# Optimization experiments

Hardware: AMD Instinct MI355X
Metric: run time of the kernel (lower is better)

## Reference

```python
import jax, jax.numpy as jnp
import numpy as np
import math

S, B, H, NH = 2048, 1, 4096, 32
HD = H // NH          # 128 head dim
ROT = HD // 2         # 64 rotary dim per half (position_encoding_2d)


def _rotary_tables(seq_len):
    inv_freq = 1.0 / (10000.0 ** (jnp.arange(0, ROT, 2, dtype=jnp.float32) / ROT))  # [ROT/2]
    t = jnp.arange(seq_len, dtype=jnp.float32)
    freqs = jnp.einsum('i,j->ij', t, inv_freq)          # [S, ROT/2]
    emb = jnp.concatenate([freqs, freqs], axis=-1)       # [S, ROT]
    return jnp.cos(emb), jnp.sin(emb)


def _rotate_half(x):
    half = x.shape[-1] // 2
    return jnp.concatenate([-x[..., half:], x[..., :half]], axis=-1)


def _apply_rotary(q, k, cos, sin, pos):
    # q,k: [s,b,nh,ROT]; pos: [s,b]
    c = cos[pos][:, :, None, :]   # [s,b,1,ROT]
    s_ = sin[pos][:, :, None, :]
    return q * c + _rotate_half(q) * s_, k * c + _rotate_half(k) * s_


def reference(hidden_states, position_ids, attention_mask, layer_id, w_qkv, b_qkv, w_dense, b_dense):
    s, b, _ = hidden_states.shape
    # fused QKV projection (Linear: x @ W.T + b)
    qkv = jnp.einsum('sbh,oh->sbo', hidden_states, w_qkv) + b_qkv     # [s,b,3H]
    qkv = qkv.reshape(s, b, NH, 3 * HD)
    q, k, v = jnp.split(qkv, 3, axis=-1)                               # each [s,b,nh,HD]
    # 2D rotary: split head dim in two halves, rotate with pos / block pos ids
    cos, sin = _rotary_tables(s)
    pos = position_ids[:, 0, :].T        # [s,b]
    blk = position_ids[:, 1, :].T        # [s,b]
    q1, q2 = jnp.split(q, 2, axis=-1)
    k1, k2 = jnp.split(k, 2, axis=-1)
    q1, k1 = _apply_rotary(q1, k1, cos, sin, pos)
    q2, k2 = _apply_rotary(q2, k2, cos, sin, blk)
    q = jnp.concatenate([q1, q2], axis=-1)
    k = jnp.concatenate([k1, k2], axis=-1)
    # layer-id-dependent scaling (GLM numerics): q scaled down by coeff, logits scaled back up
    coeff = float(layer_id + 1)
    q = q / (math.sqrt(HD) * coeff)
    scores = jnp.einsum('sbnd,tbnd->bnst', q, k)                       # [b,nh,s,s]
    scores = jnp.where(attention_mask, jnp.asarray(-10000.0, scores.dtype), scores)
    probs = jax.nn.softmax(scores.astype(jnp.float32) * coeff, axis=-1).astype(scores.dtype)
    ctx = jnp.einsum('bnst,tbnd->sbnd', probs, v).reshape(s, b, H)     # [s,b,H]
    return jnp.einsum('sbh,oh->sbo', ctx, w_dense) + b_dense


def setup_inputs() -> dict:
    key = jax.random.key(0)
    k1, k2, k3, k4, k5, k6 = jax.random.split(key, 6)
    init = 0.02
    hidden_states = jax.random.normal(k1, (S, B, H), dtype=jnp.float32)
    # GLM-style 2D position ids: [B, 2, S] (row 0: positions, row 1: block positions)
    pos = jnp.broadcast_to(jnp.arange(S, dtype=jnp.int64), (B, S))
    blk = jnp.broadcast_to(jnp.arange(S, dtype=jnp.int64), (B, S))
    position_ids = jnp.stack([pos, blk], axis=1)                        # [B,2,S]
    # causal mask: True = masked (future positions)
    causal = jnp.triu(jnp.ones((S, S), dtype=bool), k=1)
    attention_mask = jnp.broadcast_to(causal[None, None], (B, 1, S, S))
    return {
        'hidden_states': hidden_states,
        'position_ids': position_ids,
        'attention_mask': attention_mask,
        'layer_id': 5,
        'w_qkv': jax.random.normal(k2, (3 * H, H), dtype=jnp.float32) * init,
        'b_qkv': jax.random.normal(k3, (3 * H,), dtype=jnp.float32) * init,
        'w_dense': jax.random.normal(k4, (H, H), dtype=jnp.float32) * init,
        'b_dense': jax.random.normal(k5, (H,), dtype=jnp.float32) * init,
    }
```

## Files before the change

### kernel.cpp

```cpp
#include <hip/hip_runtime.h>
#include <math.h>
#include <stdint.h>

constexpr int S  = 2048;
constexpr int H  = 4096;
constexpr int NH = 32;
constexpr int HD = 128;
constexpr int H3 = 3 * H;

typedef unsigned short u16;
typedef __bf16 bf16x8 __attribute__((ext_vector_type(8)));
typedef float  f32x4  __attribute__((ext_vector_type(4)));
typedef unsigned short us8 __attribute__((ext_vector_type(8)));

__device__ __forceinline__ u16 f2bf(float f) {
  uint32_t u = __float_as_uint(f);
  uint32_t r = (u + 0x7fff + ((u >> 16) & 1)) >> 16;
  return (u16)r;
}
__device__ __forceinline__ float bf2f(u16 u) {
  return __uint_as_float((uint32_t)u << 16);
}

__device__ __forceinline__ void load_lds16(const void* g, void* l) {
  __builtin_amdgcn_global_load_lds(
      (__attribute__((address_space(1))) void*)(uintptr_t)g,
      (__attribute__((address_space(3))) void*)l,
      16, 0, 0);
}

#define SBAR0 __builtin_amdgcn_sched_barrier(0)

__global__ __launch_bounds__(256)
void cast_all(const float* __restrict__ w_qkv, const float* __restrict__ hidden,
              const float* __restrict__ w_dense, u16* __restrict__ wq,
              u16* __restrict__ hb, u16* __restrict__ wd) {
  constexpr int NQ  = H3 * H / 4;
  constexpr int NHd = S * H / 4;
  constexpr int ND  = H * H / 4;
  constexpr int NT  = NQ + NHd + ND;
  for (int i = blockIdx.x * 256 + threadIdx.x; i < NT; i += gridDim.x * 256) {
    const float4* src;
    ushort4* dst;
    int j = i;
    if (j < NQ)            { src = (const float4*)w_qkv;  dst = (ushort4*)wq; }
    else if (j < NQ + NHd) { j -= NQ; src = (const float4*)hidden; dst = (ushort4*)hb; }
    else                   { j -= NQ + NHd; src = (const float4*)w_dense; dst = (ushort4*)wd; }
    float4 v = src[j];
    ushort4 o;
    o.x = f2bf(v.x); o.y = f2bf(v.y); o.z = f2bf(v.z); o.w = f2bf(v.w);
    dst[j] = o;
  }
}

template<int NCOLS, int OUT_BF16>
__global__ __launch_bounds__(512, 2)
void gemm8p(const u16* __restrict__ A, const u16* __restrict__ W,
            const float* __restrict__ bias, void* __restrict__ Cout) {
  constexpr int K  = 4096;
  constexpr int NT = K / 64;
  constexpr int NTM = 16;
  constexpr int TB = 49152;
  __shared__ __attribute__((aligned(16))) unsigned char lds[3 * TB];
  const int tid = threadIdx.x, wave = tid >> 6, lane = tid & 63;
  const int l15 = lane & 15, l4 = lane >> 4;
  const int wr = wave >> 2, wc = wave & 3;

  const int nwg = gridDim.x, bid = blockIdx.x;
  const int cpx = nwg >> 3;
  const int swz = (bid & 7) * cpx + (bid >> 3);
  const int bx = swz / NTM, by = swz - bx * NTM;
  const int bm = by * 128, bn = bx * 256;

  const int srow = lane >> 3;
  const int sck  = ((lane & 7) ^ srow) * 8;
  const u16* Abase = A + (size_t)(bm + srow) * K + sck;
  const u16* Wbase = W + (size_t)(bn + srow) * K + sck;

  auto stageA = [&](int tt, int b) {
#pragma unroll
    for (int j = 0; j < 2; ++j) {
      const int rb = j * 64 + wave * 8;
      load_lds16(Abase + (size_t)rb * K + tt * 64, &lds[b * TB + rb * 128]);
    }
  };
  auto stageB = [&](int tt, int b, int u) {
#pragma unroll
    for (int j = 0; j < 2; ++j) {
      const int rb = u * 128 + j * 64 + wave * 8;
      load_lds16(Wbase + (size_t)rb * K + tt * 64,
                 &lds[b * TB + 16384 + rb * 128]);
    }
  };

  f32x4 acc[4][4];
#pragma unroll
  for (int i = 0; i < 4; ++i)
#pragma unroll
    for (int j = 0; j < 4; ++j) acc[i][j] = (f32x4)0.f;

  stageA(0, 0); stageB(0, 0, 0); stageB(0, 0, 1);
  stageA(1, 1); stageB(1, 1, 0); stageB(1, 1, 1);
  asm volatile("s_waitcnt vmcnt(6)" ::: "memory");
  SBAR0;
  __builtin_amdgcn_s_barrier();

  const int arow = wr * 64 + l15;
  const int brow = wc * 64 + l15;
  const int ckx  = l15 & 7;

  bf16x8 af[4][2], bf[4][2];

  int br = 0, bs = 2;
  for (int t = 0; t < NT; ++t) {
    const int b0 = br * TB;
#pragma unroll
    for (int mi = 0; mi < 2; ++mi)
#pragma unroll
      for (int ks = 0; ks < 2; ++ks)
        af[mi][ks] = *(const bf16x8*)&lds[b0 + (arow + mi * 16) * 128 +
                                          (((ks * 4 + l4) ^ ckx) * 16)];
#pragma unroll
    for (int ni = 0; ni < 2; ++ni)
#pragma unroll
      for (int ks = 0; ks < 2; ++ks)
        bf[ni][ks] = *(const bf16x8*)&lds[b0 + 16384 + (brow + ni * 16) * 128 +
                                          (((ks * 4 + l4) ^ ckx) * 16)];
    if (t < NT - 2) stageA(t + 2, bs);
    SBAR0; __builtin_amdgcn_s_barrier();
    asm volatile("s_waitcnt lgkmcnt(0)" ::: "memory");
    SBAR0;
    __builtin_amdgcn_s_setprio(1);
#pragma unroll
    for (int ks = 0; ks < 2; ++ks)
#pragma unroll
      for (int mi = 0; mi < 2; ++mi)
#pragma unroll
        for (int ni = 0; ni < 2; ++ni)
          acc[mi][ni] = __builtin_amdgcn_mfma_f32_16x16x32_bf16(af[mi][ks], bf[ni][ks], acc[mi][ni], 0, 0, 0);
    __builtin_amdgcn_s_setprio(0);
    SBAR0; __builtin_amdgcn_s_barrier();
#pragma unroll
    for (int ni = 2; ni < 4; ++ni)
#pragma unroll
      for (int ks = 0; ks < 2; ++ks)
        bf[ni][ks] = *(const bf16x8*)&lds[b0 + 16384 + (brow + ni * 16) * 128 +
                                          (((ks * 4 + l4) ^ ckx) * 16)];
    if (t < NT - 2) stageB(t + 2, bs, 0);
    SBAR0; __builtin_amdgcn_s_barrier();
    asm volatile("s_waitcnt lgkmcnt(0)" ::: "memory");
    SBAR0;
    __builtin_amdgcn_s_setprio(1);
#pragma unroll
    for (int ks = 0; ks < 2; ++ks)
#pragma unroll
      for (int mi = 0; mi < 2; ++mi)
#pragma unroll
        for (int ni = 2; ni < 4; ++ni)
          acc[mi][ni] = __builtin_amdgcn_mfma_f32_16x16x32_bf16(af[mi][ks], bf[ni][ks], acc[mi][ni], 0, 0, 0);
    __builtin_amdgcn_s_setprio(0);
    SBAR0; __builtin_amdgcn_s_barrier();
#pragma unroll
    for (int mi = 2; mi < 4; ++mi)
#pragma unroll
      for (int ks = 0; ks < 2; ++ks)
        af[mi][ks] = *(const bf16x8*)&lds[b0 + (arow + mi * 16) * 128 +
                                          (((ks * 4 + l4) ^ ckx) * 16)];
    if (t < NT - 2) stageB(t + 2, bs, 1);
    SBAR0; __builtin_amdgcn_s_barrier();
    asm volatile("s_waitcnt lgkmcnt(0)" ::: "memory");
    SBAR0;
    __builtin_amdgcn_s_setprio(1);
#pragma unroll
    for (int ks = 0; ks < 2; ++ks)
#pragma unroll
      for (int mi = 2; mi < 4; ++mi)
#pragma unroll
        for (int ni = 0; ni < 2; ++ni)
          acc[mi][ni] = __builtin_amdgcn_mfma_f32_16x16x32_bf16(af[mi][ks], bf[ni][ks], acc[mi][ni], 0, 0, 0);
    __builtin_amdgcn_s_setprio(0);
    SBAR0; __builtin_amdgcn_s_barrier();
    __builtin_amdgcn_s_setprio(1);
#pragma unroll
    for (int ks = 0; ks < 2; ++ks)
#pragma unroll
      for (int mi = 2; mi < 4; ++mi)
#pragma unroll
        for (int ni = 2; ni < 4; ++ni)
          acc[mi][ni] = __builtin_amdgcn_mfma_f32_16x16x32_bf16(af[mi][ks], bf[ni][ks], acc[mi][ni], 0, 0, 0);
    __builtin_amdgcn_s_setprio(0);
    if (t < NT - 1) {
      if (t < NT - 2) asm volatile("s_waitcnt vmcnt(6)" ::: "memory");
      else            asm volatile("s_waitcnt vmcnt(0)" ::: "memory");
      SBAR0;
      __builtin_amdgcn_s_barrier();
    }
    br = (br == 2) ? 0 : br + 1;
    bs = (bs == 2) ? 0 : bs + 1;
  }

#pragma unroll
  for (int ni = 0; ni < 4; ++ni) {
    const int col = bn + wc * 64 + ni * 16 + l15;
    const float bv = bias[col];
#pragma unroll
    for (int mi = 0; mi < 4; ++mi) {
#pragma unroll
      for (int r = 0; r < 4; ++r) {
        const int row = bm + wr * 64 + mi * 16 + l4 * 4 + r;
        const float v = acc[mi][ni][r] + bv;
        if (OUT_BF16) ((u16*)Cout)[(size_t)row * NCOLS + col] = f2bf(v);
        else          ((float*)Cout)[(size_t)row * NCOLS + col] = v;
      }
    }
  }
}

__global__ __launch_bounds__(256)
void rotary_fused(const u16* __restrict__ qkv,
                  u16* __restrict__ Qb, u16* __restrict__ Kb,
                  u16* __restrict__ Vt) {
  __shared__ u16 vt[64][136];
  __shared__ float2 cs_tab[64][32];
  const int s0 = blockIdx.x * 64, h = blockIdx.y;
  const int tid = threadIdx.x;

  for (int idx = tid; idx < 2048; idx += 256) {
    const int r = idx >> 5, j = idx & 31;
    const float invf = exp2f(-(float)j * (13.287712379549449f / 32.f));
    float sn, c;
    sincosf((float)(s0 + r) * invf, &sn, &c);
    cs_tab[r][j] = make_float2(c, sn);
  }
  for (int idx = tid; idx < 1024; idx += 256) {
    const int r = idx >> 4, ck = idx & 15;
    us8 v = *(const us8*)(qkv + (size_t)(s0 + r) * H3 + h * 384 + 256 + ck * 8);
    *(us8*)&vt[r][ck * 8] = v;
  }
  __syncthreads();

  for (int idx = tid; idx < 2048; idx += 256) {
    const int r  = idx >> 5;
    const int sub = idx & 31;
    const int tq = sub >> 4;
    const int ck = sub & 15;
    const int s = s0 + r;
    const u16* base = qkv + (size_t)s * H3 + h * 384 + tq * 128;
    us8 v = *(const us8*)(base + ck * 8);
    us8 p = *(const us8*)(base + ((ck * 8) ^ 32));
    const int d0 = ck * 8;
    const float sign = ((d0 & 63) < 32) ? -1.f : 1.f;
    const float sc = tq ? 1.f : 0.12751721769218683f;
    us8 o;
#pragma unroll
    for (int e = 0; e < 8; ++e) {
      const float2 cs = cs_tab[r][(d0 + e) & 31];
      o[e] = f2bf((bf2f(v[e]) * cs.x + sign * bf2f(p[e]) * cs.y) * sc);
    }
    *(us8*)((tq ? Kb : Qb) + ((size_t)h * S + s) * HD + d0) = o;
  }
  for (int idx = tid; idx < 1024; idx += 256) {
    const int d = idx >> 3, c8 = idx & 7;
    us8 o;
#pragma unroll
    for (int e = 0; e < 8; ++e) o[e] = vt[c8 * 8 + e][d];
    *(us8*)(Vt + ((size_t)h * HD + d) * S + s0 + c8 * 8) = o;
  }
}

__global__ __launch_bounds__(256)
void attn(const u16* __restrict__ Qb, const u16* __restrict__ Kb,
          const u16* __restrict__ Vt, u16* __restrict__ ctx) {
  __shared__ __attribute__((aligned(16))) unsigned char sK[2][64 * 256];
  __shared__ __attribute__((aligned(16))) unsigned char sV[2][128 * 128];
  __shared__ __attribute__((aligned(16))) unsigned char sP[4][16 * 128];
  const int bid = blockIdx.x;
  const int ixd = bid >> 3;
  const int h   = (bid & 7) * 4 + (ixd >> 5);
  const int qb  = 31 - (ixd & 31);
  const int tid = threadIdx.x, wave = tid >> 6, lane = tid & 63;
  const int l15 = lane & 15, l4 = lane >> 4;
  const int qw0 = qb * 64 + wave * 16;

  auto stage = [&](int it) {
    const int t0 = it * 64, b = it & 1;
#pragma unroll
    for (int c = 0; c < 4; ++c) {
      const int rbase = c * 16 + wave * 4;
      const int rr = rbase + (lane >> 4);
      const int p = lane & 15;
      load_lds16(Kb + ((size_t)h * S + t0 + rr) * HD + ((p ^ (rr & 15)) * 8),
                 &sK[b][rbase * 256]);
    }
#pragma unroll
    for (int c = 0; c < 4; ++c) {
      const int rbase = c * 32 + wave * 8;
      const int rr = rbase + (lane >> 3);
      const int p = lane & 7;
      load_lds16(Vt + ((size_t)h * HD + rr) * S + t0 + ((p ^ (rr & 7)) * 8),
                 &sV[b][rbase * 128]);
    }
  };

  bf16x8 qf[4];
  {
    const u16* qrow = Qb + ((size_t)h * S + qw0 + l15) * HD;
#pragma unroll
    for (int ks = 0; ks < 4; ++ks)
      qf[ks] = *(const bf16x8*)(qrow + ks * 32 + l4 * 8);
  }

  f32x4 of[8];
#pragma unroll
  for (int i = 0; i < 8; ++i) of[i] = (f32x4)0.f;
  float mrun[4] = {-1e30f, -1e30f, -1e30f, -1e30f};
  float lrun[4] = {0.f, 0.f, 0.f, 0.f};

  const int nt = qb + 1;
  stage(0);
  for (int it = 0; it < nt; ++it) {
    const int t0 = it * 64, b = it & 1;
    if (it + 1 < nt) {
      stage(it + 1);
      asm volatile("s_waitcnt vmcnt(8)" ::: "memory");
    } else {
      asm volatile("s_waitcnt vmcnt(0)" ::: "memory");
    }
    SBAR0;
    __builtin_amdgcn_s_barrier();
    SBAR0;

    f32x4 sc[4];
#pragma unroll
    for (int nf = 0; nf < 4; ++nf) sc[nf] = (f32x4)0.f;
#pragma unroll
    for (int nf = 0; nf < 4; ++nf) {
      const int trow = nf * 16 + l15;
#pragma unroll
      for (int ks = 0; ks < 4; ++ks) {
        const int chunk = ks * 4 + l4;
        bf16x8 kf = *(const bf16x8*)&sK[b][trow * 256 + ((chunk ^ (trow & 15)) * 16)];
        sc[nf] = __builtin_amdgcn_mfma_f32_16x16x32_bf16(qf[ks], kf, sc[nf], 0, 0, 0);
      }
    }

    if (it == qb) {
#pragma unroll
      for (int nf = 0; nf < 4; ++nf) {
        const int tg = t0 + nf * 16 + l15;
#pragma unroll
        for (int r = 0; r < 4; ++r) {
          const int sg = qw0 + l4 * 4 + r;
          if (tg > sg) sc[nf][r] = -1e30f;
        }
      }
    }

    f32x4 vm = sc[0];
#pragma unroll
    for (int nf = 1; nf < 4; ++nf)
#pragma unroll
      for (int r = 0; r < 4; ++r) vm[r] = fmaxf(vm[r], sc[nf][r]);
#pragma unroll
    for (int m = 1; m <= 8; m <<= 1)
#pragma unroll
      for (int r = 0; r < 4; ++r) vm[r] = fmaxf(vm[r], __shfl_xor(vm[r], m, 64));

    bool need = false;
#pragma unroll
    for (int r = 0; r < 4; ++r) need = need || (vm[r] > mrun[r] + 8.f);
    if (__builtin_amdgcn_ballot_w64(need)) {
#pragma unroll
      for (int r = 0; r < 4; ++r) {
        const float nm = fmaxf(mrun[r], vm[r]);
        const float scale = exp2f(mrun[r] - nm);
        mrun[r] = nm;
        lrun[r] *= scale;
#pragma unroll
        for (int i = 0; i < 8; ++i) of[i][r] *= scale;
      }
    }

    f32x4 rs = (f32x4)0.f;
#pragma unroll
    for (int nf = 0; nf < 4; ++nf) {
#pragma unroll
      for (int r = 0; r < 4; ++r) {
        const float p = exp2f(sc[nf][r] - mrun[r]);
        rs[r] += p;
        const int row = l4 * 4 + r;
        const int t = nf * 16 + l15;
        const int chunk = t >> 3;
        *(u16*)&sP[wave][row * 128 + ((chunk ^ (row & 7)) * 16) + (t & 7) * 2] = f2bf(p);
      }
    }
#pragma unroll
    for (int m = 1; m <= 8; m <<= 1)
#pragma unroll
      for (int r = 0; r < 4; ++r) rs[r] += __shfl_xor(rs[r], m, 64);
#pragma unroll
    for (int r = 0; r < 4; ++r) lrun[r] += rs[r];

    asm volatile("s_waitcnt lgkmcnt(0)" ::: "memory");
    SBAR0;

    bf16x8 pa[2];
#pragma unroll
    for (int ksP = 0; ksP < 2; ++ksP) {
      const int chunk = ksP * 4 + l4;
      pa[ksP] = *(const bf16x8*)&sP[wave][l15 * 128 + ((chunk ^ (l15 & 7)) * 16)];
    }
#pragma unroll
    for (int nf2 = 0; nf2 < 8; ++nf2) {
      const int d = nf2 * 16 + l15;
#pragma unroll
      for (int ksP = 0; ksP < 2; ++ksP) {
        const int chunk = ksP * 4 + l4;
        bf16x8 vf = *(const bf16x8*)&sV[b][d * 128 + ((chunk ^ (d & 7)) * 16)];
        of[nf2] = __builtin_amdgcn_mfma_f32_16x16x32_bf16(pa[ksP], vf, of[nf2], 0, 0, 0);
      }
    }
    SBAR0;
    __builtin_amdgcn_s_barrier();
  }

  float invr[4];
#pragma unroll
  for (int r = 0; r < 4; ++r) invr[r] = 1.f / lrun[r];
#pragma unroll
  for (int nf2 = 0; nf2 < 8; ++nf2) {
    const int d = nf2 * 16 + l15;
#pragma unroll
    for (int r = 0; r < 4; ++r) {
      const int srow = qw0 + l4 * 4 + r;
      ctx[(size_t)srow * H + h * HD + d] = f2bf(of[nf2][r] * invr[r]);
    }
  }
}

extern "C" void kernel_launch(void* const* d_in, const int* in_sizes, int n_in,
                              void* d_out, int out_size, void* d_ws, size_t ws_size,
                              hipStream_t stream) {
  (void)in_sizes; (void)n_in; (void)out_size; (void)ws_size;
  const float* hidden  = (const float*)d_in[0];
  const float* w_qkv   = (const float*)d_in[4];
  const float* b_qkv   = (const float*)d_in[5];
  const float* w_dense = (const float*)d_in[6];
  const float* b_dense = (const float*)d_in[7];
  float* out = (float*)d_out;

  char* ws = (char*)d_ws;
  u16* wqkvb   = (u16*)(ws + 0);
  u16* ctxb    = (u16*)(ws + 41943040);
  u16* wdenseb = (u16*)(ws + 58720256);
  u16* hb      = (u16*)(ws + 100663296);
  u16* qkvb    = (u16*)(ws + 117440512);
  u16* Qbp     = (u16*)(ws + 167772160);
  u16* Kbp     = (u16*)(ws + 184549376);
  u16* Vtp     = (u16*)(ws + 201326592);

  wdenseb = (u16*)(ws + 218103808);

  cast_all<<<2048, 256, 0, stream>>>(w_qkv, hidden, w_dense, wqkvb, hb, wdenseb);
  gemm8p<H3, 1><<<dim3(768), 512, 0, stream>>>(hb, wqkvb, b_qkv, qkvb);
  rotary_fused<<<dim3(S / 64, NH), 256, 0, stream>>>(qkvb, Qbp, Kbp, Vtp);
  attn<<<dim3(1024), 256, 0, stream>>>(Qbp, Kbp, Vtp, ctxb);
  gemm8p<H, 0><<<dim3(256), 512, 0, stream>>>(ctxb, wdenseb, b_dense, out);
}
```

Before: 488.8 us.

## Split QKV GEMM into 256x256-tile kernel plus 128x256 remainder kernel

Adds a gemm256 kernel that computes 256x256 output tiles with a double-buffered LDS pipeline and interleaved MFMA/load phases. It covers the first 8192 QKV columns with 256 workgroups, and the existing 128x256 gemm8p covers the remaining 4096 columns. The larger tiles raise arithmetic intensity and cut redundant global loads. The cost is two sequential launches, and each one fills only one wave of 256 workgroups, which may leave some CUs idle or tail-imbalanced.

```diff
diff --git a/kernel.cpp b/kernel.cpp
--- a/kernel.cpp
+++ b/kernel.cpp
@@ -53,7 +53,165 @@
   }
 }
 
-template<int NCOLS, int OUT_BF16>
+template<int STRIDE, int OUT_BF16>
+__global__ __launch_bounds__(512, 2)
+void gemm256(const u16* __restrict__ A, const u16* __restrict__ W,
+             const float* __restrict__ bias, void* __restrict__ Cout) {
+  constexpr int K   = 4096;
+  constexpr int NT  = K / 64;
+  constexpr int NTM = 8;
+  constexpr int TB  = 65536;
+  __shared__ __attribute__((aligned(16))) unsigned char lds[2 * TB];
+  const int tid = threadIdx.x, wave = tid >> 6, lane = tid & 63;
+  const int l15 = lane & 15, l4 = lane >> 4;
+  const int wr = wave >> 2, wc = wave & 3;
+
+  const int nwg = gridDim.x, bid = blockIdx.x;
+  const int cpx = nwg >> 3;
+  const int swz = (bid & 7) * cpx + (bid >> 3);
+  const int bx = swz / NTM, by = swz - bx * NTM;
+  const int bm = by * 256, bn = bx * 256;
+
+  const int srow = lane >> 3;
+  const int sck  = ((lane & 7) ^ srow) * 8;
+  const u16* Abase = A + (size_t)(bm + srow) * K + sck;
+  const u16* Wbase = W + (size_t)(bn + srow) * K + sck;
+
+  auto stageU = [&](int tt, int u) {
+    const int b = tt & 1;
+    if (u < 4) {
+      const int rb = u * 64 + wave * 8;
+      load_lds16(Abase + (size_t)rb * K + tt * 64, &lds[b * TB + rb * 128]);
+    } else {
+      const int rb = (u - 4) * 64 + wave * 8;
+      load_lds16(Wbase + (size_t)rb * K + tt * 64,
+                 &lds[b * TB + 32768 + rb * 128]);
+    }
+  };
+
+  f32x4 acc[8][4];
+#pragma unroll
+  for (int i = 0; i < 8; ++i)
+#pragma unroll
+    for (int j = 0; j < 4; ++j) acc[i][j] = (f32x4)0.f;
+
+#pragma unroll
+  for (int u = 0; u < 8; ++u) stageU(0, u);
+#pragma unroll
+  for (int u = 0; u < 8; ++u) stageU(1, u);
+  asm volatile("s_waitcnt vmcnt(8)" ::: "memory");
+  SBAR0;
+  __builtin_amdgcn_s_barrier();
+
+  const int arow = wr * 128 + l15;
+  const int brow = wc * 64 + l15;
+  const int ckx  = l15 & 7;
+
+  bf16x8 af[4][2], bfA[2][2], bfB[2][2];
+
+  for (int t = 0; t < NT; ++t) {
+    const int b0 = (t & 1) * TB;
+    const bool st = (t + 2 < NT);
+#pragma unroll
+    for (int mi = 0; mi < 4; ++mi)
+#pragma unroll
+      for (int ks = 0; ks < 2; ++ks)
+        af[mi][ks] = *(const bf16x8*)&lds[b0 + (arow + mi * 16) * 128 +
+                                          (((ks * 4 + l4) ^ ckx) * 16)];
+#pragma unroll
+    for (int ni = 0; ni < 2; ++ni)
+#pragma unroll
+      for (int ks = 0; ks < 2; ++ks)
+        bfA[ni][ks] = *(const bf16x8*)&lds[b0 + 32768 + (brow + ni * 16) * 128 +
+                                           (((ks * 4 + l4) ^ ckx) * 16)];
+    SBAR0; __builtin_amdgcn_s_barrier();
+    asm volatile("s_waitcnt lgkmcnt(0)" ::: "memory");
+    SBAR0;
+    __builtin_amdgcn_s_setprio(1);
+#pragma unroll
+    for (int ks = 0; ks < 2; ++ks)
+#pragma unroll
+      for (int mi = 0; mi < 4; ++mi)
+#pragma unroll
+        for (int ni = 0; ni < 2; ++ni)
+          acc[mi][ni] = __builtin_amdgcn_mfma_f32_16x16x32_bf16(af[mi][ks], bfA[ni][ks], acc[mi][ni], 0, 0, 0);
+    __builtin_amdgcn_s_setprio(0);
+    SBAR0; __builtin_amdgcn_s_barrier();
+#pragma unroll
+    for (int ni = 0; ni < 2; ++ni)
+#pragma unroll
+      for (int ks = 0; ks < 2; ++ks)
+        bfB[ni][ks] = *(const bf16x8*)&lds[b0 + 32768 + (brow + (ni + 2) * 16) * 128 +
+                                           (((ks * 4 + l4) ^ ckx) * 16)];
+    if (st) { stageU(t + 2, 0); stageU(t + 2, 2); }
+    SBAR0; __builtin_amdgcn_s_barrier();
+    asm volatile("s_waitcnt lgkmcnt(0)" ::: "memory");
+    SBAR0;
+    __builtin_amdgcn_s_setprio(1);
+#pragma unroll
+    for (int ks = 0; ks < 2; ++ks)
+#pragma unroll
+      for (int mi = 0; mi < 4; ++mi)
+#pragma unroll
+        for (int ni = 0; ni < 2; ++ni)
+          acc[mi][ni + 2] = __builtin_amdgcn_mfma_f32_16x16x32_bf16(af[mi][ks], bfB[ni][ks], acc[mi][ni + 2], 0, 0, 0);
+    __builtin_amdgcn_s_setprio(0);
+    SBAR0; __builtin_amdgcn_s_barrier();
+#pragma unroll
+    for (int mi = 0; mi < 4; ++mi)
+#pragma unroll
+      for (int ks = 0; ks < 2; ++ks)
+        af[mi][ks] = *(const bf16x8*)&lds[b0 + (arow + (mi + 4) * 16) * 128 +
+                                          (((ks * 4 + l4) ^ ckx) * 16)];
+    if (st) { stageU(t + 2, 4); stageU(t + 2, 5); }
+    SBAR0; __builtin_amdgcn_s_barrier();
+    asm volatile("s_waitcnt lgkmcnt(0)" ::: "memory");
+    SBAR0;
+    __builtin_amdgcn_s_setprio(1);
+#pragma unroll
+    for (int ks = 0; ks < 2; ++ks)
+#pragma unroll
+      for (int mi = 0; mi < 4; ++mi)
+#pragma unroll
+        for (int ni = 0; ni < 2; ++ni)
+          acc[mi + 4][ni] = __builtin_amdgcn_mfma_f32_16x16x32_bf16(af[mi][ks], bfA[ni][ks], acc[mi + 4][ni], 0, 0, 0);
+    __builtin_amdgcn_s_setprio(0);
+    SBAR0; __builtin_amdgcn_s_barrier();
+    if (st) { stageU(t + 2, 1); stageU(t + 2, 3); stageU(t + 2, 6); stageU(t + 2, 7); }
+    SBAR0;
+    __builtin_amdgcn_s_setprio(1);
+#pragma unroll
+    for (int ks = 0; ks < 2; ++ks)
+#pragma unroll
+      for (int mi = 0; mi < 4; ++mi)
+#pragma unroll
+        for (int ni = 0; ni < 2; ++ni)
+          acc[mi + 4][ni + 2] = __builtin_amdgcn_mfma_f32_16x16x32_bf16(af[mi][ks], bfB[ni][ks], acc[mi + 4][ni + 2], 0, 0, 0);
+    __builtin_amdgcn_s_setprio(0);
+    if (t < NT - 2)       asm volatile("s_waitcnt vmcnt(8)" ::: "memory");
+    else if (t == NT - 2) asm volatile("s_waitcnt vmcnt(0)" ::: "memory");
+    SBAR0;
+    if (t < NT - 1) __builtin_amdgcn_s_barrier();
+  }
+
+#pragma unroll
+  for (int ni = 0; ni < 4; ++ni) {
+    const int col = bn + wc * 64 + ni * 16 + l15;
+    const float bv = bias[col];
+#pragma unroll
+    for (int mi = 0; mi < 8; ++mi) {
+#pragma unroll
+      for (int r = 0; r < 4; ++r) {
+        const int row = bm + wr * 128 + mi * 16 + l4 * 4 + r;
+        const float v = acc[mi][ni][r] + bv;
+        if (OUT_BF16) ((u16*)Cout)[(size_t)row * STRIDE + col] = f2bf(v);
+        else          ((float*)Cout)[(size_t)row * STRIDE + col] = v;
+      }
+    }
+  }
+}
+
+template<int STRIDE, int OUT_BF16>
 __global__ __launch_bounds__(512, 2)
 void gemm8p(const u16* __restrict__ A, const u16* __restrict__ W,
             const float* __restrict__ bias, void* __restrict__ Cout) {
@@ -209,8 +367,8 @@
       for (int r = 0; r < 4; ++r) {
         const int row = bm + wr * 64 + mi * 16 + l4 * 4 + r;
         const float v = acc[mi][ni][r] + bv;
-        if (OUT_BF16) ((u16*)Cout)[(size_t)row * NCOLS + col] = f2bf(v);
-        else          ((float*)Cout)[(size_t)row * NCOLS + col] = v;
+        if (OUT_BF16) ((u16*)Cout)[(size_t)row * STRIDE + col] = f2bf(v);
+        else          ((float*)Cout)[(size_t)row * STRIDE + col] = v;
       }
     }
   }
@@ -452,17 +610,17 @@
   char* ws = (char*)d_ws;
   u16* wqkvb   = (u16*)(ws + 0);
   u16* ctxb    = (u16*)(ws + 41943040);
-  u16* wdenseb = (u16*)(ws + 58720256);
   u16* hb      = (u16*)(ws + 100663296);
   u16* qkvb    = (u16*)(ws + 117440512);
   u16* Qbp     = (u16*)(ws + 167772160);
   u16* Kbp     = (u16*)(ws + 184549376);
   u16* Vtp     = (u16*)(ws + 201326592);
-
-  wdenseb = (u16*)(ws + 218103808);
+  u16* wdenseb = (u16*)(ws + 218103808);
 
   cast_all<<<2048, 256, 0, stream>>>(w_qkv, hidden, w_dense, wqkvb, hb, wdenseb);
-  gemm8p<H3, 1><<<dim3(768), 512, 0, stream>>>(hb, wqkvb, b_qkv, qkvb);
+  gemm256<H3, 1><<<dim3(256), 512, 0, stream>>>(hb, wqkvb, b_qkv, qkvb);
+  gemm8p<H3, 1><<<dim3(256), 512, 0, stream>>>(
+      hb, wqkvb + (size_t)8192 * 4096, b_qkv + 8192, (u16*)qkvb + 8192);
   rotary_fused<<<dim3(S / 64, NH), 256, 0, stream>>>(qkvb, Qbp, Kbp, Vtp);
   attn<<<dim3(1024), 256, 0, stream>>>(Qbp, Kbp, Vtp, ctxb);
   gemm8p<H, 0><<<dim3(256), 512, 0, stream>>>(ctxb, wdenseb, b_dense, out);
```

Result: faster. 471.9 us (-3.4%).
